# Performance work log

Measured on AMD Instinct MI355X. Metric: run time of the kernel, lower is better.

Reference implementation:

```python
import jax, jax.numpy as jnp
import numpy as np

B, L, H = 8192, 64, 128
DEPTH = 3
EPS = 1e-5


def setup_inputs() -> dict:
    key = jax.random.key(0)
    ks = jax.random.split(key, 1 + 6)
    hidden_states = jax.random.normal(ks[0], (B, L, H), dtype=jnp.float32)
    # stacked per-layer params: Linear(H,H) -> LayerNorm(H) -> ReLU -> Linear(H, H//2)
    s1 = 1.0 / np.sqrt(H)
    W1 = jax.random.uniform(ks[1], (DEPTH, H, H), jnp.float32, -s1, s1)
    b1 = jax.random.uniform(ks[2], (DEPTH, H), jnp.float32, -s1, s1)
    gamma = jnp.ones((DEPTH, H), jnp.float32)
    beta = jnp.zeros((DEPTH, H), jnp.float32)
    W2 = jax.random.uniform(ks[3], (DEPTH, H, H // 2), jnp.float32, -s1, s1)
    b2 = jax.random.uniform(ks[4], (DEPTH, H // 2), jnp.float32, -s1, s1)
    return {
        "hidden_states": hidden_states,
        "W1": W1, "b1": b1, "gamma": gamma, "beta": beta,
        "W2": W2, "b2": b2,
        "lengths": L,
    }


def _layernorm(x, g, b):
    mu = jnp.mean(x, axis=-1, keepdims=True)
    var = jnp.mean(jnp.square(x - mu), axis=-1, keepdims=True)
    return (x - mu) * jax.lax.rsqrt(var + EPS) * g + b


def reference(hidden_states, W1, b1, gamma, beta, W2, b2, lengths):
    # hidden_states: [B, L, H]; max(lengths) == L
    x = hidden_states
    for i in range(DEPTH):
        h = jnp.einsum('blh,hk->blk', x, W1[i]) + b1[i]          # [B, L, H]
        h = jax.nn.relu(_layernorm(h, gamma[i], beta[i]))
        x1 = jnp.einsum('blh,hk->blk', h, W2[i]) + b2[i]          # [B, L, H//2]
        x2 = jnp.max(x1, axis=1, keepdims=True)                   # max-pool over seq
        x2 = jnp.broadcast_to(x2, x1.shape)                       # repeat to L
        x = jnp.concatenate([x1, x2], axis=2)                     # [B, L, H]
    return jnp.max(x, axis=1)                                     # [B, H]
```

## Files before the change

### kernel.cpp

```cpp
#include <hip/hip_runtime.h>

#define NB 8192
#define NL 64
#define NH 128

typedef __bf16 bf16x8 __attribute__((ext_vector_type(8)));
typedef float f32x4 __attribute__((ext_vector_type(4)));
typedef float f32x2 __attribute__((ext_vector_type(2)));
typedef unsigned uint4v __attribute__((ext_vector_type(4)));
typedef unsigned short ushort8 __attribute__((ext_vector_type(8)));

__device__ __host__ __forceinline__ int p2l(int p) {
  return (p & ~31) + ((p & 1) << 4) + ((p & 31) >> 1);
}
__device__ __host__ __forceinline__ int pi2(int p) {
  return (p & 1) ? 64 + (p >> 1) : (p >> 1);
}

__device__ __forceinline__ unsigned pk2(float lo, float hi) {
  union { __bf16 b[2]; unsigned u; } t;
  t.b[0] = (__bf16)lo; t.b[1] = (__bf16)hi;
  return t.u;
}

__global__ __launch_bounds__(256) void repack_w(const float* __restrict__ W1,
                                                const float* __restrict__ W2,
                                                const float* __restrict__ gamma,
                                                const float* __restrict__ beta,
                                                unsigned short* __restrict__ wp1,
                                                unsigned short* __restrict__ wp2,
                                                float* __restrict__ gbt) {
  int t = blockIdx.x * 256 + threadIdx.x;
  int lane = t & 63, g = t >> 6;
  if (g < 96) {
    int layer = g >> 5, rem = g & 31, nt = rem >> 2, ks = rem & 3;
    int n = nt * 16 + (lane & 15);
    int kb = ks * 32 + (lane >> 4) * 8;
    ushort8 v;
#pragma unroll
    for (int r = 0; r < 8; ++r) {
      int k = kb + r;
      int srck = (layer == 0) ? k : pi2(k);
      union { __bf16 b; unsigned short u; } c;
      c.b = (__bf16)W1[(layer * 128 + srck) * 128 + n];
      v[r] = c.u;
    }
    *reinterpret_cast<ushort8*>(wp1 + ((size_t)g * 64 + lane) * 8) = v;
  } else if (g < 144) {
    int g2 = g - 96;
    int layer = g2 >> 4, rem = g2 & 15, nt = rem >> 2, ks = rem & 3;
    int n = nt * 16 + (lane & 15);
    int kb = ks * 32 + (lane >> 4) * 8;
    ushort8 v;
#pragma unroll
    for (int r = 0; r < 8; ++r) {
      union { __bf16 b; unsigned short u; } c;
      c.b = (__bf16)W2[(layer * 128 + p2l(kb + r)) * 64 + n];
      v[r] = c.u;
    }
    *reinterpret_cast<ushort8*>(wp2 + ((size_t)g2 * 64 + lane) * 8) = v;
  } else if (g < 150) {
    int g2 = g - 144;
    int layer = g2 >> 1, param = g2 & 1;
    const float* src = (param == 0 ? gamma : beta) + layer * 128;
    float* dst = gbt + layer * 288 + param * 144;
    int p0 = lane * 2;
#pragma unroll
    for (int u = 0; u < 2; ++u) {
      int p = p0 + u;
      dst[(p >> 5) * 36 + (p & 31)] = src[p2l(p)];
    }
  }
}

__global__ __launch_bounds__(256) void fused_mlp(
    const float* __restrict__ hidden,
    const float* __restrict__ b1,
    const float* __restrict__ b2,
    const unsigned short* __restrict__ wp1u,
    const unsigned short* __restrict__ wp2u,
    const float* __restrict__ gbt,
    float* __restrict__ out) {
  __shared__ __align__(16) unsigned short xAu[NL * NH];
  __shared__ __align__(16) unsigned short xBu[NL * NH];
  __shared__ __align__(16) float gbuf[864];

  const int tid = threadIdx.x;
  const int wave = tid >> 6, lane = tid & 63;
  const int ci = lane & 15, lg = lane >> 4;
  char* xA = reinterpret_cast<char*>(xAu);
  char* xB = reinterpret_cast<char*>(xBu);

  const int abase = ci * 256;
  const int axor = ci << 4;
  const int wbase = ci * 256 + ((wave * 64 + lg * 16) ^ axor);

  if (tid < 96) {
#pragma unroll
    for (int u = 0; u < 9; ++u) gbuf[tid * 9 + u] = gbt[tid * 9 + u];
  }

  const float* src = hidden + (size_t)blockIdx.x * (NL * NH);
#pragma unroll
  for (int i = 0; i < 4; ++i) {
    int f = i * 256 + tid;
    int row = f >> 4;
    int cb = (f & 15) * 16;
    const float4* p = reinterpret_cast<const float4*>(src + f * 8);
    float4 a = p[0], bq = p[1];
    bf16x8 v;
    v[0] = (__bf16)a.x;  v[1] = (__bf16)a.y;  v[2] = (__bf16)a.z;  v[3] = (__bf16)a.w;
    v[4] = (__bf16)bq.x; v[5] = (__bf16)bq.y; v[6] = (__bf16)bq.z; v[7] = (__bf16)bq.w;
    *reinterpret_cast<bf16x8*>(xA + row * 256 + (cb ^ ((row & 15) << 4))) = v;
  }
  __syncthreads();

  for (int layer = 0; layer < 3; ++layer) {
    const unsigned short* wl1 = wp1u + (size_t)layer * 16384;
    bf16x8 w1f[2][4];
#pragma unroll
    for (int nt2 = 0; nt2 < 2; ++nt2)
#pragma unroll
      for (int ks = 0; ks < 4; ++ks)
        w1f[nt2][ks] = *reinterpret_cast<const bf16x8*>(
            wl1 + (((wave * 2 + nt2) * 4 + ks) * 64 + lane) * 8);
    f32x4 bA = *reinterpret_cast<const f32x4*>(b1 + layer * 128 + wave * 32 + lg * 4);
    f32x4 bB = *reinterpret_cast<const f32x4*>(b1 + layer * 128 + wave * 32 + 16 + lg * 4);
    f32x4 acc[4][2];
#pragma unroll
    for (int mt = 0; mt < 4; ++mt) { acc[mt][0] = bA; acc[mt][1] = bB; }
#pragma unroll
    for (int ks = 0; ks < 4; ++ks) {
      int cbx = ((ks * 64 + lg * 16) ^ axor) + abase;
#pragma unroll
      for (int mt = 0; mt < 4; ++mt) {
        bf16x8 xf = *reinterpret_cast<const bf16x8*>(xA + mt * 4096 + cbx);
        acc[mt][0] = __builtin_amdgcn_mfma_f32_16x16x32_bf16(w1f[0][ks], xf, acc[mt][0], 0, 0, 0);
        acc[mt][1] = __builtin_amdgcn_mfma_f32_16x16x32_bf16(w1f[1][ks], xf, acc[mt][1], 0, 0, 0);
      }
    }
#pragma unroll
    for (int mt = 0; mt < 4; ++mt) {
      uint4v w;
#pragma unroll
      for (int r = 0; r < 4; ++r) w[r] = pk2(acc[mt][0][r], acc[mt][1][r]);
      *reinterpret_cast<uint4v*>(xB + mt * 4096 + wbase) = w;
    }
    __syncthreads();

    {
      const int row = wave * 16 + (lane >> 2);
      const int q = lane & 3;
      const int rb = row * 256, rx = (lane >> 2) << 4;
      bf16x8 h0 = *reinterpret_cast<const bf16x8*>(xB + rb + ((q * 64 + 0) ^ rx));
      bf16x8 h1 = *reinterpret_cast<const bf16x8*>(xB + rb + ((q * 64 + 16) ^ rx));
      bf16x8 h2 = *reinterpret_cast<const bf16x8*>(xB + rb + ((q * 64 + 32) ^ rx));
      bf16x8 h3 = *reinterpret_cast<const bf16x8*>(xB + rb + ((q * 64 + 48) ^ rx));
      f32x2 f[16];
#pragma unroll
      for (int cch = 0; cch < 4; ++cch) {
        bf16x8 hv = (cch == 0) ? h0 : (cch == 1) ? h1 : (cch == 2) ? h2 : h3;
#pragma unroll
        for (int j2 = 0; j2 < 4; ++j2)
          f[cch * 4 + j2] = f32x2{(float)hv[j2 * 2], (float)hv[j2 * 2 + 1]};
      }
      f32x2 s2 = {0.f, 0.f}, q2 = {0.f, 0.f};
#pragma unroll
      for (int i = 0; i < 16; ++i) { s2 += f[i]; q2 += f[i] * f[i]; }
      float s = s2.x + s2.y, sq = q2.x + q2.y;
      s += __shfl_xor(s, 1);  sq += __shfl_xor(sq, 1);
      s += __shfl_xor(s, 2);  sq += __shfl_xor(sq, 2);
      float mu = s * (1.f / 128.f);
      float var = sq * (1.f / 128.f) - mu * mu;
      float rs = rsqrtf(var + 1e-5f);
      const f32x2* gl = reinterpret_cast<const f32x2*>(gbuf + layer * 288 + q * 36);
      const f32x2* bl = reinterpret_cast<const f32x2*>(gbuf + layer * 288 + 144 + q * 36);
#pragma unroll
      for (int cch = 0; cch < 4; ++cch) {
        union { unsigned u[4]; bf16x8 v; } yy;
#pragma unroll
        for (int j2 = 0; j2 < 4; ++j2) {
          int i = cch * 4 + j2;
          f32x2 a2 = gl[i] * rs;
          f32x2 c2 = bl[i] - a2 * mu;
          f32x2 y2 = f[i] * a2 + c2;
          yy.u[j2] = pk2(fmaxf(y2.x, 0.f), fmaxf(y2.y, 0.f));
        }
        *reinterpret_cast<bf16x8*>(xB + rb + ((q * 64 + cch * 16) ^ rx)) = yy.v;
      }
    }
    __syncthreads();

    const unsigned short* wl2 = wp2u + (size_t)layer * 8192;
    bf16x8 w2f[4];
#pragma unroll
    for (int ks = 0; ks < 4; ++ks)
      w2f[ks] = *reinterpret_cast<const bf16x8*>(
          wl2 + ((wave * 4 + ks) * 64 + lane) * 8);
    f32x4 b2v = *reinterpret_cast<const f32x4*>(b2 + layer * 64 + wave * 16 + lg * 4);
    f32x4 acc2[4];
#pragma unroll
    for (int mt = 0; mt < 4; ++mt) acc2[mt] = b2v;
#pragma unroll
    for (int ks = 0; ks < 4; ++ks) {
      int cbx = ((ks * 64 + lg * 16) ^ axor) + abase;
#pragma unroll
      for (int mt = 0; mt < 4; ++mt) {
        bf16x8 xf = *reinterpret_cast<const bf16x8*>(xB + mt * 4096 + cbx);
        acc2[mt] = __builtin_amdgcn_mfma_f32_16x16x32_bf16(w2f[ks], xf, acc2[mt], 0, 0, 0);
      }
    }

    f32x4 mm;
#pragma unroll
    for (int r = 0; r < 4; ++r)
      mm[r] = fmaxf(fmaxf(acc2[0][r], acc2[1][r]), fmaxf(acc2[2][r], acc2[3][r]));
#pragma unroll
    for (int o = 1; o < 16; o <<= 1)
#pragma unroll
      for (int r = 0; r < 4; ++r) mm[r] = fmaxf(mm[r], __shfl_xor(mm[r], o));

    if (layer < 2) {
#pragma unroll
      for (int mt = 0; mt < 4; ++mt) {
        uint4v w;
#pragma unroll
        for (int r = 0; r < 4; ++r) w[r] = pk2(acc2[mt][r], mm[r]);
        *reinterpret_cast<uint4v*>(xA + mt * 4096 + wbase) = w;
      }
      __syncthreads();
    } else {
      if (ci == 0) {
        float* o = out + (size_t)blockIdx.x * 128 + wave * 16 + lg * 4;
        *reinterpret_cast<f32x4*>(o) = mm;
        *reinterpret_cast<f32x4*>(o + 64) = mm;
      }
    }
  }
}

extern "C" void kernel_launch(void* const* d_in, const int* in_sizes, int n_in,
                              void* d_out, int out_size, void* d_ws, size_t ws_size,
                              hipStream_t stream) {
  const float* hidden = (const float*)d_in[0];
  const float* W1 = (const float*)d_in[1];
  const float* b1 = (const float*)d_in[2];
  const float* gamma = (const float*)d_in[3];
  const float* beta = (const float*)d_in[4];
  const float* W2 = (const float*)d_in[5];
  const float* b2 = (const float*)d_in[6];
  (void)in_sizes; (void)n_in; (void)out_size; (void)ws_size;

  unsigned short* wp1 = (unsigned short*)d_ws;
  unsigned short* wp2 = wp1 + 3 * 8 * 4 * 64 * 8;
  float* gbt = (float*)(wp2 + 3 * 4 * 4 * 64 * 8);
  float* out = (float*)d_out;

  repack_w<<<38, 256, 0, stream>>>(W1, W2, gamma, beta, wp1, wp2, gbt);
  fused_mlp<<<NB, 256, 0, stream>>>(hidden, b1, b2, wp1, wp2, gbt, out);
}
```

Baseline: 157.3 us.

## Process each sequence with a single wave, removing block barriers

New measurement: 270.6 us. 1.72x slower.

```diff
diff --git a/kernel.cpp b/kernel.cpp
--- a/kernel.cpp
+++ b/kernel.cpp
@@ -6,7 +6,6 @@
 
 typedef __bf16 bf16x8 __attribute__((ext_vector_type(8)));
 typedef float f32x4 __attribute__((ext_vector_type(4)));
-typedef float f32x2 __attribute__((ext_vector_type(2)));
 typedef unsigned uint4v __attribute__((ext_vector_type(4)));
 typedef unsigned short ushort8 __attribute__((ext_vector_type(8)));
 
@@ -25,11 +24,8 @@
 
 __global__ __launch_bounds__(256) void repack_w(const float* __restrict__ W1,
                                                 const float* __restrict__ W2,
-                                                const float* __restrict__ gamma,
-                                                const float* __restrict__ beta,
                                                 unsigned short* __restrict__ wp1,
-                                                unsigned short* __restrict__ wp2,
-                                                float* __restrict__ gbt) {
+                                                unsigned short* __restrict__ wp2) {
   int t = blockIdx.x * 256 + threadIdx.x;
   int lane = t & 63, g = t >> 6;
   if (g < 96) {
@@ -59,51 +55,30 @@
       v[r] = c.u;
     }
     *reinterpret_cast<ushort8*>(wp2 + ((size_t)g2 * 64 + lane) * 8) = v;
-  } else if (g < 150) {
-    int g2 = g - 144;
-    int layer = g2 >> 1, param = g2 & 1;
-    const float* src = (param == 0 ? gamma : beta) + layer * 128;
-    float* dst = gbt + layer * 288 + param * 144;
-    int p0 = lane * 2;
-#pragma unroll
-    for (int u = 0; u < 2; ++u) {
-      int p = p0 + u;
-      dst[(p >> 5) * 36 + (p & 31)] = src[p2l(p)];
-    }
   }
 }
 
-__global__ __launch_bounds__(256) void fused_mlp(
+__global__ __launch_bounds__(64) void fused_mlp(
     const float* __restrict__ hidden,
     const float* __restrict__ b1,
     const float* __restrict__ b2,
+    const float* __restrict__ gamma,
+    const float* __restrict__ beta,
     const unsigned short* __restrict__ wp1u,
     const unsigned short* __restrict__ wp2u,
-    const float* __restrict__ gbt,
     float* __restrict__ out) {
-  __shared__ __align__(16) unsigned short xAu[NL * NH];
-  __shared__ __align__(16) unsigned short xBu[NL * NH];
-  __shared__ __align__(16) float gbuf[864];
-
-  const int tid = threadIdx.x;
-  const int wave = tid >> 6, lane = tid & 63;
+  __shared__ __align__(16) unsigned short xbuf[NL * NH];
+  const int lane = threadIdx.x;
   const int ci = lane & 15, lg = lane >> 4;
-  char* xA = reinterpret_cast<char*>(xAu);
-  char* xB = reinterpret_cast<char*>(xBu);
-
-  const int abase = ci * 256;
-  const int axor = ci << 4;
-  const int wbase = ci * 256 + ((wave * 64 + lg * 16) ^ axor);
-
-  if (tid < 96) {
-#pragma unroll
-    for (int u = 0; u < 9; ++u) gbuf[tid * 9 + u] = gbt[tid * 9 + u];
-  }
+  char* xc = reinterpret_cast<char*>(xbuf);
+
+  const int rbase = ci * 256;
+  const int rxor = ci << 4;
 
   const float* src = hidden + (size_t)blockIdx.x * (NL * NH);
-#pragma unroll
-  for (int i = 0; i < 4; ++i) {
-    int f = i * 256 + tid;
+#pragma unroll 1
+  for (int i = 0; i < 16; ++i) {
+    int f = i * 64 + lane;
     int row = f >> 4;
     int cb = (f & 15) * 16;
     const float4* p = reinterpret_cast<const float4*>(src + f * 8);
@@ -111,130 +86,147 @@
     bf16x8 v;
     v[0] = (__bf16)a.x;  v[1] = (__bf16)a.y;  v[2] = (__bf16)a.z;  v[3] = (__bf16)a.w;
     v[4] = (__bf16)bq.x; v[5] = (__bf16)bq.y; v[6] = (__bf16)bq.z; v[7] = (__bf16)bq.w;
-    *reinterpret_cast<bf16x8*>(xA + row * 256 + (cb ^ ((row & 15) << 4))) = v;
+    *reinterpret_cast<bf16x8*>(xc + row * 256 + (cb ^ ((row & 15) << 4))) = v;
   }
-  __syncthreads();
-
+
+#pragma unroll 1
   for (int layer = 0; layer < 3; ++layer) {
     const unsigned short* wl1 = wp1u + (size_t)layer * 16384;
-    bf16x8 w1f[2][4];
-#pragma unroll
-    for (int nt2 = 0; nt2 < 2; ++nt2)
-#pragma unroll
-      for (int ks = 0; ks < 4; ++ks)
-        w1f[nt2][ks] = *reinterpret_cast<const bf16x8*>(
-            wl1 + (((wave * 2 + nt2) * 4 + ks) * 64 + lane) * 8);
-    f32x4 bA = *reinterpret_cast<const f32x4*>(b1 + layer * 128 + wave * 32 + lg * 4);
-    f32x4 bB = *reinterpret_cast<const f32x4*>(b1 + layer * 128 + wave * 32 + 16 + lg * 4);
-    f32x4 acc[4][2];
-#pragma unroll
-    for (int mt = 0; mt < 4; ++mt) { acc[mt][0] = bA; acc[mt][1] = bB; }
-#pragma unroll
-    for (int ks = 0; ks < 4; ++ks) {
-      int cbx = ((ks * 64 + lg * 16) ^ axor) + abase;
-#pragma unroll
-      for (int mt = 0; mt < 4; ++mt) {
-        bf16x8 xf = *reinterpret_cast<const bf16x8*>(xA + mt * 4096 + cbx);
-        acc[mt][0] = __builtin_amdgcn_mfma_f32_16x16x32_bf16(w1f[0][ks], xf, acc[mt][0], 0, 0, 0);
-        acc[mt][1] = __builtin_amdgcn_mfma_f32_16x16x32_bf16(w1f[1][ks], xf, acc[mt][1], 0, 0, 0);
-      }
-    }
-#pragma unroll
-    for (int mt = 0; mt < 4; ++mt) {
-      uint4v w;
-#pragma unroll
-      for (int r = 0; r < 4; ++r) w[r] = pk2(acc[mt][0][r], acc[mt][1][r]);
-      *reinterpret_cast<uint4v*>(xB + mt * 4096 + wbase) = w;
-    }
-    __syncthreads();
-
-    {
-      const int row = wave * 16 + (lane >> 2);
-      const int q = lane & 3;
-      const int rb = row * 256, rx = (lane >> 2) << 4;
-      bf16x8 h0 = *reinterpret_cast<const bf16x8*>(xB + rb + ((q * 64 + 0) ^ rx));
-      bf16x8 h1 = *reinterpret_cast<const bf16x8*>(xB + rb + ((q * 64 + 16) ^ rx));
-      bf16x8 h2 = *reinterpret_cast<const bf16x8*>(xB + rb + ((q * 64 + 32) ^ rx));
-      bf16x8 h3 = *reinterpret_cast<const bf16x8*>(xB + rb + ((q * 64 + 48) ^ rx));
-      f32x2 f[16];
-#pragma unroll
-      for (int cch = 0; cch < 4; ++cch) {
-        bf16x8 hv = (cch == 0) ? h0 : (cch == 1) ? h1 : (cch == 2) ? h2 : h3;
-#pragma unroll
-        for (int j2 = 0; j2 < 4; ++j2)
-          f[cch * 4 + j2] = f32x2{(float)hv[j2 * 2], (float)hv[j2 * 2 + 1]};
-      }
-      f32x2 s2 = {0.f, 0.f}, q2 = {0.f, 0.f};
-#pragma unroll
-      for (int i = 0; i < 16; ++i) { s2 += f[i]; q2 += f[i] * f[i]; }
-      float s = s2.x + s2.y, sq = q2.x + q2.y;
-      s += __shfl_xor(s, 1);  sq += __shfl_xor(sq, 1);
-      s += __shfl_xor(s, 2);  sq += __shfl_xor(sq, 2);
-      float mu = s * (1.f / 128.f);
-      float var = sq * (1.f / 128.f) - mu * mu;
-      float rs = rsqrtf(var + 1e-5f);
-      const f32x2* gl = reinterpret_cast<const f32x2*>(gbuf + layer * 288 + q * 36);
-      const f32x2* bl = reinterpret_cast<const f32x2*>(gbuf + layer * 288 + 144 + q * 36);
-#pragma unroll
-      for (int cch = 0; cch < 4; ++cch) {
-        union { unsigned u[4]; bf16x8 v; } yy;
-#pragma unroll
-        for (int j2 = 0; j2 < 4; ++j2) {
-          int i = cch * 4 + j2;
-          f32x2 a2 = gl[i] * rs;
-          f32x2 c2 = bl[i] - a2 * mu;
-          f32x2 y2 = f[i] * a2 + c2;
-          yy.u[j2] = pk2(fmaxf(y2.x, 0.f), fmaxf(y2.y, 0.f));
-        }
-        *reinterpret_cast<bf16x8*>(xB + rb + ((q * 64 + cch * 16) ^ rx)) = yy.v;
-      }
-    }
-    __syncthreads();
-
-    const unsigned short* wl2 = wp2u + (size_t)layer * 8192;
-    bf16x8 w2f[4];
-#pragma unroll
-    for (int ks = 0; ks < 4; ++ks)
-      w2f[ks] = *reinterpret_cast<const bf16x8*>(
-          wl2 + ((wave * 4 + ks) * 64 + lane) * 8);
-    f32x4 b2v = *reinterpret_cast<const f32x4*>(b2 + layer * 64 + wave * 16 + lg * 4);
-    f32x4 acc2[4];
-#pragma unroll
-    for (int mt = 0; mt < 4; ++mt) acc2[mt] = b2v;
-#pragma unroll
-    for (int ks = 0; ks < 4; ++ks) {
-      int cbx = ((ks * 64 + lg * 16) ^ axor) + abase;
-#pragma unroll
-      for (int mt = 0; mt < 4; ++mt) {
-        bf16x8 xf = *reinterpret_cast<const bf16x8*>(xB + mt * 4096 + cbx);
-        acc2[mt] = __builtin_amdgcn_mfma_f32_16x16x32_bf16(w2f[ks], xf, acc2[mt], 0, 0, 0);
-      }
-    }
-
-    f32x4 mm;
-#pragma unroll
-    for (int r = 0; r < 4; ++r)
-      mm[r] = fmaxf(fmaxf(acc2[0][r], acc2[1][r]), fmaxf(acc2[2][r], acc2[3][r]));
-#pragma unroll
-    for (int o = 1; o < 16; o <<= 1)
-#pragma unroll
-      for (int r = 0; r < 4; ++r) mm[r] = fmaxf(mm[r], __shfl_xor(mm[r], o));
-
-    if (layer < 2) {
+
+    uint4v hpk[4][4];
+    float sum[4], sq[4];
+#pragma unroll
+    for (int mt = 0; mt < 4; ++mt) { sum[mt] = 0.f; sq[mt] = 0.f; }
+
+#pragma unroll
+    for (int c = 0; c < 4; ++c) {
+      bf16x8 w1f0[4], w1f1[4];
+#pragma unroll
+      for (int ks = 0; ks < 4; ++ks) {
+        w1f0[ks] = *reinterpret_cast<const bf16x8*>(
+            wl1 + (((c * 2 + 0) * 4 + ks) * 64 + lane) * 8);
+        w1f1[ks] = *reinterpret_cast<const bf16x8*>(
+            wl1 + (((c * 2 + 1) * 4 + ks) * 64 + lane) * 8);
+      }
+      f32x4 bA = *reinterpret_cast<const f32x4*>(b1 + layer * 128 + c * 32 + lg * 4);
+      f32x4 bB = *reinterpret_cast<const f32x4*>(b1 + layer * 128 + c * 32 + 16 + lg * 4);
+      f32x4 acc0[4], acc1[4];
+#pragma unroll
+      for (int mt = 0; mt < 4; ++mt) { acc0[mt] = bA; acc1[mt] = bB; }
+#pragma unroll
+      for (int ks = 0; ks < 4; ++ks) {
+        int cbx = ((ks * 64 + lg * 16) ^ rxor) + rbase;
+#pragma unroll
+        for (int mt = 0; mt < 4; ++mt) {
+          bf16x8 xf = *reinterpret_cast<const bf16x8*>(xc + mt * 4096 + cbx);
+          acc0[mt] = __builtin_amdgcn_mfma_f32_16x16x32_bf16(w1f0[ks], xf, acc0[mt], 0, 0, 0);
+          acc1[mt] = __builtin_amdgcn_mfma_f32_16x16x32_bf16(w1f1[ks], xf, acc1[mt], 0, 0, 0);
+        }
+      }
 #pragma unroll
       for (int mt = 0; mt < 4; ++mt) {
         uint4v w;
 #pragma unroll
-        for (int r = 0; r < 4; ++r) w[r] = pk2(acc2[mt][r], mm[r]);
-        *reinterpret_cast<uint4v*>(xA + mt * 4096 + wbase) = w;
-      }
-      __syncthreads();
-    } else {
-      if (ci == 0) {
-        float* o = out + (size_t)blockIdx.x * 128 + wave * 16 + lg * 4;
-        *reinterpret_cast<f32x4*>(o) = mm;
-        *reinterpret_cast<f32x4*>(o + 64) = mm;
-      }
+        for (int r = 0; r < 4; ++r) {
+          float a0 = acc0[mt][r], a1 = acc1[mt][r];
+          sum[mt] += a0 + a1;
+          sq[mt] = fmaf(a0, a0, fmaf(a1, a1, sq[mt]));
+          w[r] = pk2(a0, a1);
+        }
+        hpk[c][mt] = w;
+      }
+    }
+
+    float mu[4], rs[4];
+#pragma unroll
+    for (int mt = 0; mt < 4; ++mt) {
+      float s = sum[mt], q = sq[mt];
+      s += __shfl_xor(s, 16);  q += __shfl_xor(q, 16);
+      s += __shfl_xor(s, 32);  q += __shfl_xor(q, 32);
+      mu[mt] = s * (1.f / 128.f);
+      float var = q * (1.f / 128.f) - mu[mt] * mu[mt];
+      rs[mt] = rsqrtf(var + 1e-5f);
+    }
+
+#pragma unroll
+    for (int c = 0; c < 4; ++c) {
+      f32x4 glo = *reinterpret_cast<const f32x4*>(gamma + layer * 128 + c * 32 + lg * 4);
+      f32x4 ghi = *reinterpret_cast<const f32x4*>(gamma + layer * 128 + c * 32 + 16 + lg * 4);
+      f32x4 tlo = *reinterpret_cast<const f32x4*>(beta + layer * 128 + c * 32 + lg * 4);
+      f32x4 thi = *reinterpret_cast<const f32x4*>(beta + layer * 128 + c * 32 + 16 + lg * 4);
+#pragma unroll
+      for (int mt = 0; mt < 4; ++mt) {
+        f32x4 alo = glo * rs[mt], ahi = ghi * rs[mt];
+        f32x4 clo = tlo - alo * mu[mt], chi = thi - ahi * mu[mt];
+        uint4v hw = hpk[c][mt], w;
+#pragma unroll
+        for (int r = 0; r < 4; ++r) {
+          unsigned u = hw[r];
+          float lo = __uint_as_float(u << 16);
+          float hi = __uint_as_float(u & 0xffff0000u);
+          float ylo = fmaxf(fmaf(lo, alo[r], clo[r]), 0.f);
+          float yhi = fmaxf(fmaf(hi, ahi[r], chi[r]), 0.f);
+          w[r] = pk2(ylo, yhi);
+        }
+        *reinterpret_cast<uint4v*>(
+            xc + mt * 4096 + rbase + ((c * 64 + lg * 16) ^ rxor)) = w;
+      }
+    }
+
+    const unsigned short* wl2 = wp2u + (size_t)layer * 8192;
+    uint4v xpk[4][4];
+#pragma unroll
+    for (int c2 = 0; c2 < 4; ++c2) {
+      bf16x8 w2f[4];
+#pragma unroll
+      for (int ks = 0; ks < 4; ++ks)
+        w2f[ks] = *reinterpret_cast<const bf16x8*>(
+            wl2 + ((c2 * 4 + ks) * 64 + lane) * 8);
+      f32x4 b2v = *reinterpret_cast<const f32x4*>(b2 + layer * 64 + c2 * 16 + lg * 4);
+      f32x4 acc2[4];
+#pragma unroll
+      for (int mt = 0; mt < 4; ++mt) acc2[mt] = b2v;
+#pragma unroll
+      for (int ks = 0; ks < 4; ++ks) {
+        int cbx = ((ks * 64 + lg * 16) ^ rxor) + rbase;
+#pragma unroll
+        for (int mt = 0; mt < 4; ++mt) {
+          bf16x8 xf = *reinterpret_cast<const bf16x8*>(xc + mt * 4096 + cbx);
+          acc2[mt] = __builtin_amdgcn_mfma_f32_16x16x32_bf16(w2f[ks], xf, acc2[mt], 0, 0, 0);
+        }
+      }
+      f32x4 mm;
+#pragma unroll
+      for (int r = 0; r < 4; ++r)
+        mm[r] = fmaxf(fmaxf(acc2[0][r], acc2[1][r]), fmaxf(acc2[2][r], acc2[3][r]));
+#pragma unroll
+      for (int o = 1; o < 16; o <<= 1)
+#pragma unroll
+        for (int r = 0; r < 4; ++r) mm[r] = fmaxf(mm[r], __shfl_xor(mm[r], o));
+
+      if (layer < 2) {
+#pragma unroll
+        for (int mt = 0; mt < 4; ++mt) {
+          uint4v w;
+#pragma unroll
+          for (int r = 0; r < 4; ++r) w[r] = pk2(acc2[mt][r], mm[r]);
+          xpk[c2][mt] = w;
+        }
+      } else {
+        if (ci == 0) {
+          float* o = out + (size_t)blockIdx.x * 128 + c2 * 16 + lg * 4;
+          *reinterpret_cast<f32x4*>(o) = mm;
+          *reinterpret_cast<f32x4*>(o + 64) = mm;
+        }
+      }
+    }
+    if (layer < 2) {
+#pragma unroll
+      for (int c2 = 0; c2 < 4; ++c2)
+#pragma unroll
+        for (int mt = 0; mt < 4; ++mt)
+          *reinterpret_cast<uint4v*>(
+              xc + mt * 4096 + rbase + ((c2 * 64 + lg * 16) ^ rxor)) = xpk[c2][mt];
     }
   }
 }
@@ -253,9 +245,8 @@
 
   unsigned short* wp1 = (unsigned short*)d_ws;
   unsigned short* wp2 = wp1 + 3 * 8 * 4 * 64 * 8;
-  float* gbt = (float*)(wp2 + 3 * 4 * 4 * 64 * 8);
   float* out = (float*)d_out;
 
-  repack_w<<<38, 256, 0, stream>>>(W1, W2, gamma, beta, wp1, wp2, gbt);
-  fused_mlp<<<NB, 256, 0, stream>>>(hidden, b1, b2, wp1, wp2, gbt, out);
-}
+  repack_w<<<36, 256, 0, stream>>>(W1, W2, wp1, wp2);
+  fused_mlp<<<NB, 64, 0, stream>>>(hidden, b1, b2, gamma, beta, wp1, wp2, out);
+}
```

## Fuse LayerNorm into first GEMM epilogue using cross-wave LDS partial sums

Applied to the files above, without the earlier changes.

Measured after the change: 159.0 us. No clear change (+1.1%).

```diff
diff --git a/kernel.cpp b/kernel.cpp
--- a/kernel.cpp
+++ b/kernel.cpp
@@ -1,12 +1,9 @@
 #include <hip/hip_runtime.h>
 
 #define NB 8192
-#define NL 64
-#define NH 128
 
 typedef __bf16 bf16x8 __attribute__((ext_vector_type(8)));
 typedef float f32x4 __attribute__((ext_vector_type(4)));
-typedef float f32x2 __attribute__((ext_vector_type(2)));
 typedef unsigned uint4v __attribute__((ext_vector_type(4)));
 typedef unsigned short ushort8 __attribute__((ext_vector_type(8)));
 
@@ -25,11 +22,8 @@
 
 __global__ __launch_bounds__(256) void repack_w(const float* __restrict__ W1,
                                                 const float* __restrict__ W2,
-                                                const float* __restrict__ gamma,
-                                                const float* __restrict__ beta,
                                                 unsigned short* __restrict__ wp1,
-                                                unsigned short* __restrict__ wp2,
-                                                float* __restrict__ gbt) {
+                                                unsigned short* __restrict__ wp2) {
   int t = blockIdx.x * 256 + threadIdx.x;
   int lane = t & 63, g = t >> 6;
   if (g < 96) {
@@ -59,17 +53,6 @@
       v[r] = c.u;
     }
     *reinterpret_cast<ushort8*>(wp2 + ((size_t)g2 * 64 + lane) * 8) = v;
-  } else if (g < 150) {
-    int g2 = g - 144;
-    int layer = g2 >> 1, param = g2 & 1;
-    const float* src = (param == 0 ? gamma : beta) + layer * 128;
-    float* dst = gbt + layer * 288 + param * 144;
-    int p0 = lane * 2;
-#pragma unroll
-    for (int u = 0; u < 2; ++u) {
-      int p = p0 + u;
-      dst[(p >> 5) * 36 + (p & 31)] = src[p2l(p)];
-    }
   }
 }
 
@@ -77,13 +60,15 @@
     const float* __restrict__ hidden,
     const float* __restrict__ b1,
     const float* __restrict__ b2,
+    const float* __restrict__ gamma,
+    const float* __restrict__ beta,
     const unsigned short* __restrict__ wp1u,
     const unsigned short* __restrict__ wp2u,
-    const float* __restrict__ gbt,
     float* __restrict__ out) {
-  __shared__ __align__(16) unsigned short xAu[NL * NH];
-  __shared__ __align__(16) unsigned short xBu[NL * NH];
-  __shared__ __align__(16) float gbuf[864];
+  __shared__ __align__(16) unsigned short xAu[64 * 128];
+  __shared__ __align__(16) unsigned short xBu[64 * 128];
+  __shared__ __align__(16) float ssum[4][64];
+  __shared__ __align__(16) float qsum[4][64];
 
   const int tid = threadIdx.x;
   const int wave = tid >> 6, lane = tid & 63;
@@ -91,16 +76,11 @@
   char* xA = reinterpret_cast<char*>(xAu);
   char* xB = reinterpret_cast<char*>(xBu);
 
-  const int abase = ci * 256;
-  const int axor = ci << 4;
-  const int wbase = ci * 256 + ((wave * 64 + lg * 16) ^ axor);
-
-  if (tid < 96) {
-#pragma unroll
-    for (int u = 0; u < 9; ++u) gbuf[tid * 9 + u] = gbt[tid * 9 + u];
-  }
-
-  const float* src = hidden + (size_t)blockIdx.x * (NL * NH);
+  const int rbase = ci * 256;
+  const int rxor = ci << 4;
+  const int wbase = ci * 256 + ((wave * 64 + lg * 16) ^ rxor);
+
+  const float* src = hidden + (size_t)blockIdx.x * (64 * 128);
 #pragma unroll
   for (int i = 0; i < 4; ++i) {
     int f = i * 256 + tid;
@@ -108,22 +88,16 @@
     int cb = (f & 15) * 16;
     const float4* p = reinterpret_cast<const float4*>(src + f * 8);
     float4 a = p[0], bq = p[1];
-    bf16x8 v;
-    v[0] = (__bf16)a.x;  v[1] = (__bf16)a.y;  v[2] = (__bf16)a.z;  v[3] = (__bf16)a.w;
-    v[4] = (__bf16)bq.x; v[5] = (__bf16)bq.y; v[6] = (__bf16)bq.z; v[7] = (__bf16)bq.w;
-    *reinterpret_cast<bf16x8*>(xA + row * 256 + (cb ^ ((row & 15) << 4))) = v;
+    uint4v v;
+    v[0] = pk2(a.x, a.y);  v[1] = pk2(a.z, a.w);
+    v[2] = pk2(bq.x, bq.y); v[3] = pk2(bq.z, bq.w);
+    *reinterpret_cast<uint4v*>(xA + row * 256 + (cb ^ ((row & 15) << 4))) = v;
   }
   __syncthreads();
 
+#pragma unroll 1
   for (int layer = 0; layer < 3; ++layer) {
     const unsigned short* wl1 = wp1u + (size_t)layer * 16384;
-    bf16x8 w1f[2][4];
-#pragma unroll
-    for (int nt2 = 0; nt2 < 2; ++nt2)
-#pragma unroll
-      for (int ks = 0; ks < 4; ++ks)
-        w1f[nt2][ks] = *reinterpret_cast<const bf16x8*>(
-            wl1 + (((wave * 2 + nt2) * 4 + ks) * 64 + lane) * 8);
     f32x4 bA = *reinterpret_cast<const f32x4*>(b1 + layer * 128 + wave * 32 + lg * 4);
     f32x4 bB = *reinterpret_cast<const f32x4*>(b1 + layer * 128 + wave * 32 + 16 + lg * 4);
     f32x4 acc[4][2];
@@ -131,83 +105,84 @@
     for (int mt = 0; mt < 4; ++mt) { acc[mt][0] = bA; acc[mt][1] = bB; }
 #pragma unroll
     for (int ks = 0; ks < 4; ++ks) {
-      int cbx = ((ks * 64 + lg * 16) ^ axor) + abase;
+      bf16x8 bf0 = *reinterpret_cast<const bf16x8*>(
+          wl1 + (((wave * 2 + 0) * 4 + ks) * 64 + lane) * 8);
+      bf16x8 bf1 = *reinterpret_cast<const bf16x8*>(
+          wl1 + (((wave * 2 + 1) * 4 + ks) * 64 + lane) * 8);
+      int cbx = ((ks * 64 + lg * 16) ^ rxor) + rbase;
 #pragma unroll
       for (int mt = 0; mt < 4; ++mt) {
         bf16x8 xf = *reinterpret_cast<const bf16x8*>(xA + mt * 4096 + cbx);
-        acc[mt][0] = __builtin_amdgcn_mfma_f32_16x16x32_bf16(w1f[0][ks], xf, acc[mt][0], 0, 0, 0);
-        acc[mt][1] = __builtin_amdgcn_mfma_f32_16x16x32_bf16(w1f[1][ks], xf, acc[mt][1], 0, 0, 0);
-      }
-    }
-#pragma unroll
-    for (int mt = 0; mt < 4; ++mt) {
-      uint4v w;
-#pragma unroll
-      for (int r = 0; r < 4; ++r) w[r] = pk2(acc[mt][0][r], acc[mt][1][r]);
-      *reinterpret_cast<uint4v*>(xB + mt * 4096 + wbase) = w;
+        acc[mt][0] = __builtin_amdgcn_mfma_f32_16x16x32_bf16(bf0, xf, acc[mt][0], 0, 0, 0);
+        acc[mt][1] = __builtin_amdgcn_mfma_f32_16x16x32_bf16(bf1, xf, acc[mt][1], 0, 0, 0);
+      }
+    }
+
+    {
+      float s[4], q[4];
+#pragma unroll
+      for (int mt = 0; mt < 4; ++mt) {
+        f32x4 a0 = acc[mt][0], a1 = acc[mt][1];
+        f32x4 ss = a0 + a1;
+        f32x4 qq = a0 * a0 + a1 * a1;
+        s[mt] = (ss[0] + ss[1]) + (ss[2] + ss[3]);
+        q[mt] = (qq[0] + qq[1]) + (qq[2] + qq[3]);
+      }
+#pragma unroll
+      for (int mt = 0; mt < 4; ++mt) {
+        s[mt] += __shfl_xor(s[mt], 16);  q[mt] += __shfl_xor(q[mt], 16);
+        s[mt] += __shfl_xor(s[mt], 32);  q[mt] += __shfl_xor(q[mt], 32);
+      }
+      if (lane < 16) {
+#pragma unroll
+        for (int mt = 0; mt < 4; ++mt) {
+          ssum[wave][mt * 16 + lane] = s[mt];
+          qsum[wave][mt * 16 + lane] = q[mt];
+        }
+      }
     }
     __syncthreads();
 
     {
-      const int row = wave * 16 + (lane >> 2);
-      const int q = lane & 3;
-      const int rb = row * 256, rx = (lane >> 2) << 4;
-      bf16x8 h0 = *reinterpret_cast<const bf16x8*>(xB + rb + ((q * 64 + 0) ^ rx));
-      bf16x8 h1 = *reinterpret_cast<const bf16x8*>(xB + rb + ((q * 64 + 16) ^ rx));
-      bf16x8 h2 = *reinterpret_cast<const bf16x8*>(xB + rb + ((q * 64 + 32) ^ rx));
-      bf16x8 h3 = *reinterpret_cast<const bf16x8*>(xB + rb + ((q * 64 + 48) ^ rx));
-      f32x2 f[16];
-#pragma unroll
-      for (int cch = 0; cch < 4; ++cch) {
-        bf16x8 hv = (cch == 0) ? h0 : (cch == 1) ? h1 : (cch == 2) ? h2 : h3;
-#pragma unroll
-        for (int j2 = 0; j2 < 4; ++j2)
-          f[cch * 4 + j2] = f32x2{(float)hv[j2 * 2], (float)hv[j2 * 2 + 1]};
-      }
-      f32x2 s2 = {0.f, 0.f}, q2 = {0.f, 0.f};
-#pragma unroll
-      for (int i = 0; i < 16; ++i) { s2 += f[i]; q2 += f[i] * f[i]; }
-      float s = s2.x + s2.y, sq = q2.x + q2.y;
-      s += __shfl_xor(s, 1);  sq += __shfl_xor(sq, 1);
-      s += __shfl_xor(s, 2);  sq += __shfl_xor(sq, 2);
-      float mu = s * (1.f / 128.f);
-      float var = sq * (1.f / 128.f) - mu * mu;
-      float rs = rsqrtf(var + 1e-5f);
-      const f32x2* gl = reinterpret_cast<const f32x2*>(gbuf + layer * 288 + q * 36);
-      const f32x2* bl = reinterpret_cast<const f32x2*>(gbuf + layer * 288 + 144 + q * 36);
-#pragma unroll
-      for (int cch = 0; cch < 4; ++cch) {
-        union { unsigned u[4]; bf16x8 v; } yy;
-#pragma unroll
-        for (int j2 = 0; j2 < 4; ++j2) {
-          int i = cch * 4 + j2;
-          f32x2 a2 = gl[i] * rs;
-          f32x2 c2 = bl[i] - a2 * mu;
-          f32x2 y2 = f[i] * a2 + c2;
-          yy.u[j2] = pk2(fmaxf(y2.x, 0.f), fmaxf(y2.y, 0.f));
+      f32x4 glo = *reinterpret_cast<const f32x4*>(gamma + layer * 128 + wave * 32 + lg * 4);
+      f32x4 ghi = *reinterpret_cast<const f32x4*>(gamma + layer * 128 + wave * 32 + 16 + lg * 4);
+      f32x4 tlo = *reinterpret_cast<const f32x4*>(beta + layer * 128 + wave * 32 + lg * 4);
+      f32x4 thi = *reinterpret_cast<const f32x4*>(beta + layer * 128 + wave * 32 + 16 + lg * 4);
+#pragma unroll
+      for (int mt = 0; mt < 4; ++mt) {
+        int L = mt * 16 + ci;
+        float sf = (ssum[0][L] + ssum[1][L]) + (ssum[2][L] + ssum[3][L]);
+        float qf = (qsum[0][L] + qsum[1][L]) + (qsum[2][L] + qsum[3][L]);
+        float mu = sf * (1.f / 128.f);
+        float rs = rsqrtf(qf * (1.f / 128.f) - mu * mu + 1e-5f);
+        f32x4 alo = glo * rs, ahi = ghi * rs;
+        f32x4 clo = tlo - alo * mu, chi = thi - ahi * mu;
+        uint4v w;
+#pragma unroll
+        for (int r = 0; r < 4; ++r) {
+          float ylo = fmaxf(fmaf(acc[mt][0][r], alo[r], clo[r]), 0.f);
+          float yhi = fmaxf(fmaf(acc[mt][1][r], ahi[r], chi[r]), 0.f);
+          w[r] = pk2(ylo, yhi);
         }
-        *reinterpret_cast<bf16x8*>(xB + rb + ((q * 64 + cch * 16) ^ rx)) = yy.v;
+        *reinterpret_cast<uint4v*>(xB + mt * 4096 + wbase) = w;
       }
     }
     __syncthreads();
 
     const unsigned short* wl2 = wp2u + (size_t)layer * 8192;
-    bf16x8 w2f[4];
-#pragma unroll
-    for (int ks = 0; ks < 4; ++ks)
-      w2f[ks] = *reinterpret_cast<const bf16x8*>(
-          wl2 + ((wave * 4 + ks) * 64 + lane) * 8);
     f32x4 b2v = *reinterpret_cast<const f32x4*>(b2 + layer * 64 + wave * 16 + lg * 4);
     f32x4 acc2[4];
 #pragma unroll
     for (int mt = 0; mt < 4; ++mt) acc2[mt] = b2v;
 #pragma unroll
     for (int ks = 0; ks < 4; ++ks) {
-      int cbx = ((ks * 64 + lg * 16) ^ axor) + abase;
+      bf16x8 wf = *reinterpret_cast<const bf16x8*>(
+          wl2 + ((wave * 4 + ks) * 64 + lane) * 8);
+      int cbx = ((ks * 64 + lg * 16) ^ rxor) + rbase;
 #pragma unroll
       for (int mt = 0; mt < 4; ++mt) {
         bf16x8 xf = *reinterpret_cast<const bf16x8*>(xB + mt * 4096 + cbx);
-        acc2[mt] = __builtin_amdgcn_mfma_f32_16x16x32_bf16(w2f[ks], xf, acc2[mt], 0, 0, 0);
+        acc2[mt] = __builtin_amdgcn_mfma_f32_16x16x32_bf16(wf, xf, acc2[mt], 0, 0, 0);
       }
     }
 
@@ -253,9 +228,8 @@
 
   unsigned short* wp1 = (unsigned short*)d_ws;
   unsigned short* wp2 = wp1 + 3 * 8 * 4 * 64 * 8;
-  float* gbt = (float*)(wp2 + 3 * 4 * 4 * 64 * 8);
   float* out = (float*)d_out;
 
-  repack_w<<<38, 256, 0, stream>>>(W1, W2, gamma, beta, wp1, wp2, gbt);
-  fused_mlp<<<NB, 256, 0, stream>>>(hidden, b1, b2, wp1, wp2, gbt, out);
-}
+  repack_w<<<36, 256, 0, stream>>>(W1, W2, wp1, wp2);
+  fused_mlp<<<NB, 256, 0, stream>>>(hidden, b1, b2, gamma, beta, wp1, wp2, out);
+}
```
